# Optimization experiments

Measured on AMD Instinct MI355X. Metric: run time of the kernel, lower is better.

## Reference

```python
import jax, jax.numpy as jnp
import numpy as np

NEG_SLOPE = 0.01


def conv2d_border(x, w, b, stride):
    # replicate ('border') padding of 1, then VALID conv; matches torch padding_mode='border'
    x = jnp.pad(x, ((0, 0), (0, 0), (1, 1), (1, 1)), mode='edge')
    y = jax.lax.conv_general_dilated(x, w, (stride, stride), 'VALID',
                                     dimension_numbers=('NCHW', 'OIHW', 'NCHW'))
    return y + b[None, :, None, None]


def leaky(x):
    return jnp.where(x >= 0, x, NEG_SLOPE * x)


def view_encoder(x, w1, b1, w2, b2, w3, b3):
    x = leaky(conv2d_border(x, w1, b1, 1))
    x = leaky(conv2d_border(x, w2, b2, 2))
    x = leaky(conv2d_border(x, w3, b3, 2))
    return x  # (V, F, H/4, W/4)


def bilinear_gather(nts, uv, vid):
    # nts: (V, F, Hp, Wp); uv: (N, 2) in [0,1]; vid: (N,) int -> (N, F)
    V, Fd, Hp, Wp = nts.shape
    tex = jnp.transpose(nts, (0, 2, 3, 1))  # (V, Hp, Wp, F)
    x = uv[:, 0] * (Wp - 1)
    y = uv[:, 1] * (Hp - 1)
    x0 = jnp.clip(jnp.floor(x).astype(jnp.int32), 0, Wp - 2)
    y0 = jnp.clip(jnp.floor(y).astype(jnp.int32), 0, Hp - 2)
    wx = (x - x0)[:, None]
    wy = (y - y0)[:, None]
    f00 = tex[vid, y0, x0]
    f01 = tex[vid, y0, x0 + 1]
    f10 = tex[vid, y0 + 1, x0]
    f11 = tex[vid, y0 + 1, x0 + 1]
    return (f00 * (1 - wx) * (1 - wy) + f01 * wx * (1 - wy)
            + f10 * (1 - wx) * wy + f11 * wx * wy)


def mha(q, k, v, wq, bq, wk, bk, wv, bv, wo, bo, num_heads):
    # q: (B,1,D), k/v: (B,S,D); torch nn.MultiheadAttention math, batch_first
    B, Lq, D = q.shape
    S = k.shape[1]
    hd = D // num_heads
    qh = (q @ wq.T + bq).reshape(B, Lq, num_heads, hd).transpose(0, 2, 1, 3)
    kh = (k @ wk.T + bk).reshape(B, S, num_heads, hd).transpose(0, 2, 1, 3)
    vh = (v @ wv.T + bv).reshape(B, S, num_heads, hd).transpose(0, 2, 1, 3)
    scores = jnp.einsum('bhqd,bhkd->bhqk', qh, kh) / jnp.sqrt(jnp.float32(hd)).astype(q.dtype)
    attn = jax.nn.softmax(scores, axis=-1)
    out = jnp.einsum('bhqk,bhkd->bhqd', attn, vh)
    out = out.transpose(0, 2, 1, 3).reshape(B, Lq, D)
    return out @ wo.T + bo


def setup_inputs() -> dict:
    key = jax.random.key(0)
    ks = jax.random.split(key, 20)
    V, C, H, W = 8, 3, 512, 512
    B = 262144
    D = 64
    view_tex = jax.random.normal(ks[0], (V, C, H, W), jnp.float32)
    uv = jax.random.uniform(ks[1], (B, 3, 2), jnp.float32)
    vid = jax.random.randint(ks[2], (B, 3, 1), 0, V).astype(jnp.float32)
    uvi = jnp.concatenate([uv, vid], axis=-1)  # (B,3,3)
    raydir = jax.random.normal(ks[3], (B, 3), jnp.float32)

    def winit(k, shape, fan_in):
        return jax.random.normal(k, shape, jnp.float32) / np.sqrt(fan_in)

    params = dict(
        w1=winit(ks[4], (32, C, 3, 3), C * 9), b1=jnp.zeros((32,), jnp.float32),
        w2=winit(ks[5], (64, 32, 3, 3), 32 * 9), b2=jnp.zeros((64,), jnp.float32),
        w3=winit(ks[6], (D, 64, 3, 3), 64 * 9), b3=jnp.zeros((D,), jnp.float32),
        rw1=winit(ks[7], (64, 3), 3), rb1=jnp.zeros((64,), jnp.float32),
        rw2=winit(ks[8], (D, 64), 64), rb2=jnp.zeros((D,), jnp.float32),
        wq=winit(ks[9], (D, D), D), bq=jnp.zeros((D,), jnp.float32),
        wk=winit(ks[10], (D, D), D), bk=jnp.zeros((D,), jnp.float32),
        wv=winit(ks[11], (D, D), D), bv=jnp.zeros((D,), jnp.float32),
        wo=winit(ks[12], (D, D), D), bo=jnp.zeros((D,), jnp.float32),
    )
    return dict(view_tex=view_tex, uvi=uvi, raydir=raydir, **params)


def reference(view_tex, uvi, raydir,
              w1, b1, w2, b2, w3, b3,
              rw1, rb1, rw2, rb2,
              wq, bq, wk, bk, wv, bv, wo, bo):
    NUM_HEADS = 4
    nts = view_encoder(view_tex, w1, b1, w2, b2, w3, b3)  # (V,F,Hp,Wp)
    B = uvi.shape[0]
    uv = uvi[:, :, :2].reshape(B * 3, 2)
    vid = uvi[:, :, 2].astype(jnp.int32).reshape(B * 3)
    feats = bilinear_gather(nts, uv, vid).reshape(B, 3, -1)  # (B,3,F)
    ray_feat = jnp.maximum(raydir @ rw1.T + rb1, 0) @ rw2.T + rb2  # (B,F)
    fused = mha(ray_feat[:, None, :], feats, feats,
                wq, bq, wk, bk, wv, bv, wo, bo, NUM_HEADS)
    return fused[:, 0, :], feats
```

## Files before the change

kernel.cpp:

```cpp
#include <hip/hip_runtime.h>

typedef short s8v __attribute__((ext_vector_type(8)));
typedef short s4v __attribute__((ext_vector_type(4)));
typedef float f4v __attribute__((ext_vector_type(4)));

#define DEV __device__ __forceinline__

DEV short f2bs(float f){
  unsigned int u = __float_as_uint(f);
  u += 0x7fffu + ((u >> 16) & 1u);
  return (short)(u >> 16);
}
DEV float b2f(short s){
  return __uint_as_float(((unsigned int)(unsigned short)s) << 16);
}
DEV float lrelu(float x){ return x >= 0.f ? x : 0.01f*x; }
DEV unsigned pk2(float a, float b){
  return (unsigned)(unsigned short)f2bs(a) | ((unsigned)(unsigned short)f2bs(b) << 16);
}

__global__ __launch_bounds__(256) void k0_prep(
    const float* __restrict__ w1, const float* __restrict__ w2,
    const float* __restrict__ w3, const float* __restrict__ rw2,
    const float* __restrict__ wq, const float* __restrict__ wk,
    const float* __restrict__ wv, const float* __restrict__ wo,
    char* __restrict__ wreg)
{
  int idx = blockIdx.x*256 + threadIdx.x;
  short* w1b = (short*)(wreg);
  short* w2b = (short*)(wreg + 3456);
  short* w3b = (short*)(wreg + 40320);
  short* rw2b = (short*)(wreg + 114048);
  short* wkb  = (short*)(wreg + 130432);
  short* wvb  = (short*)(wreg + 138624);
  short* wob  = (short*)(wreg + 146816);
  if (idx < 1024){
    int e = idx & 7, l = (idx >> 3) & 63, m = idx >> 9;
    int k = (l >> 4)*8 + e;
    int cout = m*16 + (l & 15);
    w1b[idx] = (k < 27) ? f2bs(w1[cout*27 + k]) : (short)0;
  } else if (idx < 19456){
    int j = idx - 1024;
    int kk = j / 2048, c = (j >> 5) & 63, ci = j & 31;
    w2b[j] = f2bs(w2[c*288 + ci*9 + kk]);
  } else if (idx < 56320){
    int j = idx - 19456;
    int kk = j / 4096, c = (j >> 6) & 63, ci = j & 63;
    w3b[j] = f2bs(w3[c*576 + ci*9 + kk]);
  } else if (idx < 60416){
    int j = idx - 56320; rw2b[j] = f2bs(rw2[j]);
  } else if (idx < 64512){
  } else if (idx < 68608){
    int j = idx - 64512; wkb[j] = f2bs(wk[j]);
  } else if (idx < 72704){
    int j = idx - 68608; wvb[j] = f2bs(wv[j]);
  } else if (idx < 76800){
    int j = idx - 72704; wob[j] = f2bs(wo[j]);
  }
}

__global__ __launch_bounds__(256) void k0b_fold(
    const float* __restrict__ wq, const float* __restrict__ rw2,
    const float* __restrict__ rb2, const float* __restrict__ bq,
    char* __restrict__ wreg)
{
  short* wqrb = (short*)(wreg + 122240);
  float* bqr  = (float*)(wreg + 155008);
  int tid = threadIdx.x;
  int i = tid >> 2, k0 = (tid & 3)*16;
  #pragma unroll
  for (int kk=0; kk<16; kk++){
    int k = k0 + kk;
    float s = 0.f;
    #pragma unroll
    for (int j=0; j<64; j++) s += wq[i*64+j]*rw2[j*64+k];
    wqrb[i*64+k] = f2bs(s);
  }
  if (tid < 64){
    float s = bq[tid];
    #pragma unroll
    for (int j=0; j<64; j++) s += wq[tid*64+j]*rb2[j];
    bqr[tid] = s;
  }
}

__global__ __launch_bounds__(256) void kc12(
    const float* __restrict__ vt, short* __restrict__ c2,
    const short* __restrict__ w1b, const float* __restrict__ b1,
    const short* __restrict__ w2b, const float* __restrict__ b2, int v0)
{
  __shared__ short srcT[3108];
  __shared__ short rb[4][2880];
  const int tid = threadIdx.x;
  const int l = tid & 63, wid = tid >> 6;
  const int p = l & 15, g = l >> 4;
  const int yb = blockIdx.y;
  const int oyb = (yb & 7)*16 + (yb >> 3);
  const int OXB = blockIdx.x*64, OYB = oyb*2;
  const float* src = vt + (size_t)(v0 + blockIdx.z)*3*512*512;

  #pragma unroll
  for (int it=0; it<13; it++){
    int idx = it*256 + tid;
    if (idx < 3108){
      int ci = idx/1036, rem = idx - ci*1036;
      int row = rem/148, col = rem - row*148;
      int gr = min(max(2*OYB - 2 + row, 0), 511);
      int gc = min(max(2*OXB - 2 + col, 0), 511);
      srcT[idx] = f2bs(src[((size_t)ci*512 + gr)*512 + gc]);
    }
  }

  int boffB[8];
  #pragma unroll
  for (int e=0;e<8;e++){
    int k = g*8 + e;
    int ci = (k*57) >> 9;
    int r9 = k - ci*9;
    int dy = (r9*11) >> 5;
    int dx = r9 - dy*3;
    boffB[e] = (k < 27) ? (ci*1036 + dy*148 + dx) : 0;
  }
  s8v af0 = *(const s8v*)(w1b + l*8);
  s8v af1 = *(const s8v*)(w1b + 512 + l*8);
  f4v cb0 = *(const f4v*)(b1 + g*4);
  f4v cb1 = *(const f4v*)(b1 + 16 + g*4);

  const int dlt = wid >> 1, h = wid & 1;
  const int oy = OYB + dlt;
  const int ox0 = OXB + h*32;
  const int Cw0 = 2*ox0 - 1;
  short* myrb = rb[wid];
  const f4v FZ = {0.f,0.f,0.f,0.f};
  f4v acc[2][4];
  #pragma unroll
  for (int s2=0;s2<2;s2++)
    #pragma unroll
    for (int m=0;m<4;m++) acc[s2][m] = FZ;

  __syncthreads();

  #pragma unroll
  for (int ky=0; ky<3; ky++){
    const int R = min(max(2*oy + ky - 1, 0), 511);
    const int trb = R - 2*OYB + 1;
    const int sbase = trb*148 + 64*h + p;

    #pragma unroll
    for (int s=0; s<5; s++){
      s8v bf;
      #pragma unroll
      for (int e=0;e<8;e++) bf[e] = srcT[boffB[e] + sbase + s*16];
      f4v d0 = __builtin_amdgcn_mfma_f32_16x16x32_bf16(af0, bf, FZ, 0,0,0);
      f4v d1 = __builtin_amdgcn_mfma_f32_16x16x32_bf16(af1, bf, FZ, 0,0,0);
      int wcol = s*16 + p;
      uint2 wa = { pk2(lrelu(d0[0]+cb0[0]), lrelu(d0[1]+cb0[1])),
                   pk2(lrelu(d0[2]+cb0[2]), lrelu(d0[3]+cb0[3])) };
      *(uint2*)(myrb + wcol*36 + g*4) = wa;
      uint2 wb2 = { pk2(lrelu(d1[0]+cb1[0]), lrelu(d1[1]+cb1[1])),
                    pk2(lrelu(d1[2]+cb1[2]), lrelu(d1[3]+cb1[3])) };
      *(uint2*)(myrb + wcol*36 + 16 + g*4) = wb2;
    }

    #pragma unroll
    for (int s2=0; s2<2; s2++){
      const int locox = s2*16 + p;
      #pragma unroll
      for (int kx=0; kx<3; kx++){
        int raw = Cw0 + 2*locox + kx;
        int ri = max(raw, 0) - Cw0;
        uint2 lo2 = *(const uint2*)(myrb + ri*36 + g*8);
        uint2 hi2 = *(const uint2*)(myrb + ri*36 + g*8 + 4);
        uint4 t4 = {lo2.x, lo2.y, hi2.x, hi2.y};
        s8v bf2 = __builtin_bit_cast(s8v, t4);
        #pragma unroll
        for (int m=0;m<4;m++){
          s8v afr = *(const s8v*)(w2b + ((ky*3+kx)*64 + m*16 + p)*32 + g*8);
          acc[s2][m] = __builtin_amdgcn_mfma_f32_16x16x32_bf16(afr, bf2, acc[s2][m], 0,0,0);
        }
      }
    }
  }

  #pragma unroll
  for (int s2=0; s2<2; s2++){
    short* o = c2 + (((size_t)blockIdx.z*256 + oy)*256 + ox0 + s2*16 + p)*64;
    #pragma unroll
    for (int m=0;m<4;m++){
      f4v bb = *(const f4v*)(b2 + m*16 + g*4);
      s4v pk;
      #pragma unroll
      for (int r=0;r<4;r++) pk[r] = f2bs(lrelu(acc[s2][m][r] + bb[r]));
      *(s4v*)(o + m*16 + g*4) = pk;
    }
  }
}

template<int CIN, int TILES>
__global__ __launch_bounds__(256) void conv_mfma(
    const short* __restrict__ src0, short* __restrict__ dst,
    const short* __restrict__ wb, const float* __restrict__ bias,
    int IH, int IW, int OW, int dstV0)
{
  const int l = threadIdx.x & 63, w = threadIdx.x >> 6;
  const int p = l & 15, g = l >> 4;
  const int ox0 = blockIdx.x*(64*TILES) + w*(16*TILES) + p;
  const int yb = blockIdx.y;
  const int oy = (yb & 7)*16 + (yb >> 3);
  const short* src = src0 + (size_t)blockIdx.z*IH*IW*CIN;
  const f4v FZ = {0.f,0.f,0.f,0.f};
  f4v acc[TILES][4];
  #pragma unroll
  for (int tl=0;tl<TILES;tl++)
    #pragma unroll
    for (int m=0;m<4;m++) acc[tl][m] = FZ;
  #pragma unroll
  for (int ky=0;ky<3;ky++){
    int iy = min(max(2*oy+ky-1, 0), IH-1);
    #pragma unroll
    for (int kx=0;kx<3;kx++){
      #pragma unroll
      for (int ch=0; ch<CIN/32; ch++){
        s8v bfrag[TILES];
        #pragma unroll
        for (int tl=0;tl<TILES;tl++){
          int ix = min(max(2*(ox0 + 16*tl)+kx-1, 0), IW-1);
          bfrag[tl] = *(const s8v*)(src + ((size_t)iy*IW + ix)*CIN + ch*32 + g*8);
        }
        #pragma unroll
        for (int m=0;m<4;m++){
          s8v afrag = *(const s8v*)(wb + ((ky*3+kx)*64 + m*16 + p)*CIN + ch*32 + g*8);
          #pragma unroll
          for (int tl=0;tl<TILES;tl++)
            acc[tl][m] = __builtin_amdgcn_mfma_f32_16x16x32_bf16(afrag, bfrag[tl], acc[tl][m], 0,0,0);
        }
      }
    }
  }
  const int OH = gridDim.y;
  #pragma unroll
  for (int tl=0;tl<TILES;tl++){
    short* o = dst + (((size_t)(dstV0 + blockIdx.z)*OH + oy)*OW + ox0 + 16*tl)*64;
    #pragma unroll
    for (int m=0;m<4;m++){
      f4v bb = *(const f4v*)(bias + m*16 + g*4);
      s4v pk;
      #pragma unroll
      for (int r=0;r<4;r++) pk[r] = f2bs(lrelu(acc[tl][m][r] + bb[r]));
      *(s4v*)(o + m*16 + g*4) = pk;
    }
  }
}

#define AFRG(W) (*(const s8v*)((W) + (m*16 + p)*64 + kc*32 + g*8))

__global__ __launch_bounds__(256) void k45_fused(
    const short* __restrict__ nts, const float* __restrict__ uvi,
    const float* __restrict__ raydir,
    const float* __restrict__ rw1, const float* __restrict__ rb1,
    const short* __restrict__ wqrb, const float* __restrict__ bqr,
    const short* __restrict__ wkb, const float* __restrict__ bk,
    const short* __restrict__ wvb, const float* __restrict__ bv,
    const short* __restrict__ wob, const float* __restrict__ bo,
    float* __restrict__ outFused, float* __restrict__ outFeats)
{
  __shared__ short lds_fb[64*3*72];
  const int tid = threadIdx.x;
  const int l = tid & 63, wid = tid >> 6;
  const int p = l & 15, g = l >> 4;
  const int pt0 = blockIdx.x*64;
  const f4v FZ = {0.f,0.f,0.f,0.f};

  #pragma unroll
  for (int i=0; i<6; i++){
    int ck = i*256 + tid;
    int ptl = ck/24, rem = ck - ptl*24;
    int t = rem >> 3, c8 = rem & 7;
    int pt = pt0 + ptl;
    const float* up = uvi + (size_t)pt*9 + t*3;
    float u = up[0], v = up[1];
    int vid = (int)up[2];
    float xf = u*127.f, yf = v*127.f;
    int x0 = min(max((int)floorf(xf), 0), 126);
    int y0 = min(max((int)floorf(yf), 0), 126);
    float wx = xf - (float)x0, wy = yf - (float)y0;
    const short* cb = nts + ((size_t)((vid*128 + y0)*128 + x0))*64 + c8*8;
    s8v c00 = *(const s8v*)(cb);
    s8v c01 = *(const s8v*)(cb + 64);
    s8v c10 = *(const s8v*)(cb + 8192);
    s8v c11 = *(const s8v*)(cb + 8192 + 64);
    f4v o0, o1;
    s8v pk;
    #pragma unroll
    for (int e=0;e<8;e++){
      float a = b2f(c00[e]); a += wx*(b2f(c01[e]) - a);
      float b = b2f(c10[e]); b += wx*(b2f(c11[e]) - b);
      float val = a + wy*(b - a);
      if (e < 4) o0[e] = val; else o1[e-4] = val;
      pk[e] = f2bs(val);
    }
    float* op = outFeats + ((size_t)pt*3 + t)*64 + c8*8;
    *(f4v*)op = o0;
    *(f4v*)(op+4) = o1;
    *(s8v*)(&lds_fb[(ptl*3 + t)*72 + c8*8]) = pk;
  }

  __syncthreads();

  const int ptl16 = wid*16 + p;
  const int pt = pt0 + ptl16;

  s8v fb[3][2];
  #pragma unroll
  for (int t=0;t<3;t++)
    #pragma unroll
    for (int kc=0;kc<2;kc++)
      fb[t][kc] = *(const s8v*)(&lds_fb[(ptl16*3 + t)*72 + kc*32 + g*8]);

  float rd0 = raydir[(size_t)pt*3+0];
  float rd1 = raydir[(size_t)pt*3+1];
  float rd2 = raydir[(size_t)pt*3+2];
  s8v xb[2];
  #pragma unroll
  for (int kc=0;kc<2;kc++){
    s8v tmp;
    #pragma unroll
    for (int e=0;e<8;e++){
      int j = kc*32 + g*8 + e;
      float hv = fmaxf(rb1[j] + rw1[j*3]*rd0 + rw1[j*3+1]*rd1 + rw1[j*3+2]*rd2, 0.f);
      tmp[e] = f2bs(hv);
    }
    xb[kc] = tmp;
  }

  f4v acc[4];
  #pragma unroll
  for (int m=0;m<4;m++) acc[m] = FZ;
  #pragma unroll
  for (int kc=0;kc<2;kc++){
    #pragma unroll
    for (int m=0;m<4;m++)
      acc[m] = __builtin_amdgcn_mfma_f32_16x16x32_bf16(AFRG(wqrb), xb[kc], acc[m], 0,0,0);
  }
  float qh[4][4];
  #pragma unroll
  for (int m=0;m<4;m++){
    f4v bb = *(const f4v*)(bqr + m*16 + g*4);
    #pragma unroll
    for (int r=0;r<4;r++) qh[m][r] = acc[m][r] + bb[r];
  }

  s8v wkf[2][4];
  #pragma unroll
  for (int kc=0;kc<2;kc++)
    #pragma unroll
    for (int m=0;m<4;m++)
      wkf[kc][m] = AFRG(wkb);

  float sc[3][4];
  #pragma unroll
  for (int t=0;t<3;t++){
    f4v ka[4];
    #pragma unroll
    for (int m=0;m<4;m++) ka[m] = FZ;
    #pragma unroll
    for (int kc=0;kc<2;kc++){
      #pragma unroll
      for (int m=0;m<4;m++)
        ka[m] = __builtin_amdgcn_mfma_f32_16x16x32_bf16(wkf[kc][m], fb[t][kc], ka[m], 0,0,0);
    }
    #pragma unroll
    for (int m=0;m<4;m++){
      f4v bb = *(const f4v*)(bk + m*16 + g*4);
      float part = 0.f;
      #pragma unroll
      for (int r=0;r<4;r++) part += qh[m][r]*(ka[m][r] + bb[r]);
      part += __shfl_xor(part, 16, 64);
      part += __shfl_xor(part, 32, 64);
      sc[t][m] = part*0.25f;
    }
  }

  #pragma unroll
  for (int m=0;m<4;m++){
    float mx = fmaxf(fmaxf(sc[0][m], sc[1][m]), sc[2][m]);
    float e0 = __expf(sc[0][m]-mx);
    float e1 = __expf(sc[1][m]-mx);
    float e2 = __expf(sc[2][m]-mx);
    float inv = 1.f/(e0+e1+e2);
    sc[0][m] = e0*inv; sc[1][m] = e1*inv; sc[2][m] = e2*inv;
  }

  s8v wvf[2][4];
  #pragma unroll
  for (int kc=0;kc<2;kc++)
    #pragma unroll
    for (int m=0;m<4;m++)
      wvf[kc][m] = AFRG(wvb);

  float o[4][4];
  #pragma unroll
  for (int m=0;m<4;m++)
    #pragma unroll
    for (int r=0;r<4;r++) o[m][r] = 0.f;
  #pragma unroll
  for (int t=0;t<3;t++){
    f4v va[4];
    #pragma unroll
    for (int m=0;m<4;m++) va[m] = FZ;
    #pragma unroll
    for (int kc=0;kc<2;kc++){
      #pragma unroll
      for (int m=0;m<4;m++)
        va[m] = __builtin_amdgcn_mfma_f32_16x16x32_bf16(wvf[kc][m], fb[t][kc], va[m], 0,0,0);
    }
    #pragma unroll
    for (int m=0;m<4;m++)
      #pragma unroll
      for (int r=0;r<4;r++) o[m][r] += sc[t][m]*va[m][r];
  }
  #pragma unroll
  for (int m=0;m<4;m++){
    f4v bb = *(const f4v*)(bv + m*16 + g*4);
    #pragma unroll
    for (int r=0;r<4;r++) o[m][r] += bb[r];
  }

  {
    unsigned* rl = (unsigned*)lds_fb + wid*1728;
    #pragma unroll
    for (int m=0;m<4;m++){
      unsigned lo = pk2(o[m][0], o[m][1]);
      unsigned hi = pk2(o[m][2], o[m][3]);
      rl[p*36 + m*8 + g*2] = lo;
      rl[p*36 + m*8 + g*2 + 1] = hi;
    }
    xb[0] = __builtin_bit_cast(s8v, *(uint4*)(rl + p*36 + g*4));
    xb[1] = __builtin_bit_cast(s8v, *(uint4*)(rl + p*36 + 16 + g*4));
  }

  #pragma unroll
  for (int m=0;m<4;m++) acc[m] = FZ;
  #pragma unroll
  for (int kc=0;kc<2;kc++){
    #pragma unroll
    for (int m=0;m<4;m++)
      acc[m] = __builtin_amdgcn_mfma_f32_16x16x32_bf16(AFRG(wob), xb[kc], acc[m], 0,0,0);
  }
  #pragma unroll
  for (int m=0;m<4;m++){
    f4v bb = *(const f4v*)(bo + m*16 + g*4);
    f4v res;
    #pragma unroll
    for (int r=0;r<4;r++) res[r] = acc[m][r] + bb[r];
    *(f4v*)(outFused + (size_t)pt*64 + m*16 + g*4) = res;
  }
}

extern "C" void kernel_launch(void* const* d_in, const int* in_sizes, int n_in,
                              void* d_out, int out_size, void* d_ws, size_t ws_size,
                              hipStream_t stream)
{
  const float* view_tex = (const float*)d_in[0];
  const float* uvi    = (const float*)d_in[1];
  const float* raydir = (const float*)d_in[2];
  const float* w1 = (const float*)d_in[3];
  const float* b1 = (const float*)d_in[4];
  const float* w2 = (const float*)d_in[5];
  const float* b2 = (const float*)d_in[6];
  const float* w3 = (const float*)d_in[7];
  const float* b3 = (const float*)d_in[8];
  const float* rw1 = (const float*)d_in[9];
  const float* rb1 = (const float*)d_in[10];
  const float* rw2 = (const float*)d_in[11];
  const float* rb2 = (const float*)d_in[12];
  const float* wq = (const float*)d_in[13];
  const float* bq = (const float*)d_in[14];
  const float* wk = (const float*)d_in[15];
  const float* bk = (const float*)d_in[16];
  const float* wv = (const float*)d_in[17];
  const float* bv = (const float*)d_in[18];
  const float* wo = (const float*)d_in[19];
  const float* bo = (const float*)d_in[20];
  float* out = (float*)d_out;

  const int V = in_sizes[0] / (3*512*512);
  const int B = in_sizes[1] / 9;
  const size_t FEATS_OFF = (size_t)B*64;

  const size_t C2F  = (size_t)V*256*256*64*2;
  const size_t C2V  = (size_t)256*256*64*2;
  const size_t NTSB = (size_t)V*128*128*64*2;
  const size_t WREG = 262144;

  char* base = (char*)d_ws;
  bool full = (ws_size >= C2F + NTSB + WREG);

  char *c2, *ntsp, *wreg;
  if (full){
    c2 = base; ntsp = c2 + C2F; wreg = ntsp + NTSB;
  } else {
    c2 = base; ntsp = c2 + C2V; wreg = ntsp + NTSB;
  }
  short* w1b = (short*)(wreg);
  short* w2b = (short*)(wreg + 3456);
  short* w3b = (short*)(wreg + 40320);
  short* wqrb = (short*)(wreg + 122240);
  short* wkb  = (short*)(wreg + 130432);
  short* wvb  = (short*)(wreg + 138624);
  short* wob  = (short*)(wreg + 146816);
  float* bqr  = (float*)(wreg + 155008);

  k0_prep<<<dim3(300),256,0,stream>>>(w1,w2,w3,rw2,wq,wk,wv,wo,wreg);
  k0b_fold<<<dim3(1),256,0,stream>>>(wq, rw2, rb2, bq, wreg);

  if (full){
    kc12<<<dim3(4,128,V),256,0,stream>>>(view_tex,(short*)c2,w1b,b1,w2b,b2,0);
    conv_mfma<64,2><<<dim3(1,128,V),256,0,stream>>>((const short*)c2,(short*)ntsp,w3b,b3,256,256,128,0);
  } else {
    for (int v=0; v<V; v++){
      kc12<<<dim3(4,128,1),256,0,stream>>>(view_tex,(short*)c2,w1b,b1,w2b,b2,v);
      conv_mfma<64,2><<<dim3(1,128,1),256,0,stream>>>((const short*)c2,(short*)ntsp,w3b,b3,256,256,128,v);
    }
  }

  k45_fused<<<dim3(B/64),256,0,stream>>>((const short*)ntsp, uvi, raydir,
      rw1, rb1, wqrb, bqr, wkb, bk, wvb, bv, wob, bo,
      out, out + FEATS_OFF);
}
```

Before: 308.1 us.

## Sort gather tokens by view via counting sort before bilinear gather

Splits the fused gather+attention kernel into a counting-sort pass (histogram, offsets, scatter) that groups gather tokens by view id, a view-ordered bilinear gather kernel with block swizzling, and a separate attention kernel that reloads the fp32 features from global memory. The aim is better cache locality on the texture feature map during gathers. In exchange it adds several extra launches, atomics, and a round-trip of the feature tensor through global memory. The fallback path for small workspaces now always runs the full-size conv, so it is no longer memory-safe, and the scatter order is nondeterministic.

```diff
diff --git a/kernel.cpp b/kernel.cpp
--- a/kernel.cpp
+++ b/kernel.cpp
@@ -84,6 +84,87 @@
   }
 }
 
+__global__ void kzero(int* cnt){ if (threadIdx.x < 8) cnt[threadIdx.x] = 0; }
+
+__global__ __launch_bounds__(256) void kcnt(
+    const float* __restrict__ uvi, int* __restrict__ cnt)
+{
+  __shared__ int lh[8];
+  int tid = threadIdx.x;
+  if (tid < 8) lh[tid] = 0;
+  __syncthreads();
+  int tk = blockIdx.x*256 + tid;
+  int v = (int)uvi[(size_t)tk*3 + 2];
+  atomicAdd(&lh[v], 1);
+  __syncthreads();
+  if (tid < 8) atomicAdd(&cnt[tid], lh[tid]);
+}
+
+__global__ void kofs(const int* cnt, int* cur)
+{
+  if (threadIdx.x == 0){
+    int run = 0;
+    for (int v=0; v<8; v++){ cur[v] = run; run += cnt[v]; }
+  }
+}
+
+__global__ __launch_bounds__(256) void kscat(
+    const float* __restrict__ uvi, int* __restrict__ cur,
+    int* __restrict__ ord, float2* __restrict__ uvo)
+{
+  __shared__ int lh[8];
+  __shared__ int gb[8];
+  int tid = threadIdx.x;
+  if (tid < 8) lh[tid] = 0;
+  __syncthreads();
+  int tk = blockIdx.x*256 + tid;
+  float u = uvi[(size_t)tk*3];
+  float vv = uvi[(size_t)tk*3 + 1];
+  int v = (int)uvi[(size_t)tk*3 + 2];
+  int rank = atomicAdd(&lh[v], 1);
+  __syncthreads();
+  if (tid < 8) gb[tid] = atomicAdd(&cur[tid], lh[tid]);
+  __syncthreads();
+  int pos = gb[v] + rank;
+  ord[pos] = tk;
+  uvo[pos] = make_float2(u, vv);
+}
+
+__global__ __launch_bounds__(256) void k4v(
+    const short* __restrict__ nts, const int* __restrict__ ord,
+    const float2* __restrict__ uvo, float* __restrict__ outFeats, int nblk8)
+{
+  int b = blockIdx.x;
+  int swb = (b & 7)*nblk8 + (b >> 3);
+  int tid = threadIdx.x;
+  int idx = swb*32 + (tid >> 3);
+  int c8 = tid & 7;
+  int tok = ord[idx];
+  float2 uv = uvo[idx];
+  float xf = uv.x*127.f, yf = uv.y*127.f;
+  int x0 = min(max((int)floorf(xf), 0), 126);
+  int y0 = min(max((int)floorf(yf), 0), 126);
+  float wx = xf - (float)x0, wy = yf - (float)y0;
+  int vid = tok >> 24;
+  tok &= 0xFFFFFF;
+  const short* cb = nts + ((size_t)((vid*128 + y0)*128 + x0))*64 + c8*8;
+  s8v c00 = *(const s8v*)(cb);
+  s8v c01 = *(const s8v*)(cb + 64);
+  s8v c10 = *(const s8v*)(cb + 8192);
+  s8v c11 = *(const s8v*)(cb + 8192 + 64);
+  f4v o0, o1;
+  #pragma unroll
+  for (int e=0;e<8;e++){
+    float a = b2f(c00[e]); a += wx*(b2f(c01[e]) - a);
+    float b2 = b2f(c10[e]); b2 += wx*(b2f(c11[e]) - b2);
+    float val = a + wy*(b2 - a);
+    if (e < 4) o0[e] = val; else o1[e-4] = val;
+  }
+  float* op = outFeats + (size_t)tok*64 + c8*8;
+  *(f4v*)op = o0;
+  *(f4v*)(op+4) = o1;
+}
+
 __global__ __launch_bounds__(256) void kc12(
     const float* __restrict__ vt, short* __restrict__ c2,
     const short* __restrict__ w1b, const float* __restrict__ b1,
@@ -254,68 +335,36 @@
 
 #define AFRG(W) (*(const s8v*)((W) + (m*16 + p)*64 + kc*32 + g*8))
 
-__global__ __launch_bounds__(256) void k45_fused(
-    const short* __restrict__ nts, const float* __restrict__ uvi,
-    const float* __restrict__ raydir,
+__global__ __launch_bounds__(256) void k5s(
+    const float* __restrict__ feats, const float* __restrict__ raydir,
     const float* __restrict__ rw1, const float* __restrict__ rb1,
     const short* __restrict__ wqrb, const float* __restrict__ bqr,
     const short* __restrict__ wkb, const float* __restrict__ bk,
     const short* __restrict__ wvb, const float* __restrict__ bv,
     const short* __restrict__ wob, const float* __restrict__ bo,
-    float* __restrict__ outFused, float* __restrict__ outFeats)
-{
-  __shared__ short lds_fb[64*3*72];
+    float* __restrict__ outFused)
+{
+  __shared__ unsigned rlds[4][576];
   const int tid = threadIdx.x;
   const int l = tid & 63, wid = tid >> 6;
   const int p = l & 15, g = l >> 4;
-  const int pt0 = blockIdx.x*64;
+  const int pt = blockIdx.x*64 + wid*16 + p;
   const f4v FZ = {0.f,0.f,0.f,0.f};
 
-  #pragma unroll
-  for (int i=0; i<6; i++){
-    int ck = i*256 + tid;
-    int ptl = ck/24, rem = ck - ptl*24;
-    int t = rem >> 3, c8 = rem & 7;
-    int pt = pt0 + ptl;
-    const float* up = uvi + (size_t)pt*9 + t*3;
-    float u = up[0], v = up[1];
-    int vid = (int)up[2];
-    float xf = u*127.f, yf = v*127.f;
-    int x0 = min(max((int)floorf(xf), 0), 126);
-    int y0 = min(max((int)floorf(yf), 0), 126);
-    float wx = xf - (float)x0, wy = yf - (float)y0;
-    const short* cb = nts + ((size_t)((vid*128 + y0)*128 + x0))*64 + c8*8;
-    s8v c00 = *(const s8v*)(cb);
-    s8v c01 = *(const s8v*)(cb + 64);
-    s8v c10 = *(const s8v*)(cb + 8192);
-    s8v c11 = *(const s8v*)(cb + 8192 + 64);
-    f4v o0, o1;
-    s8v pk;
-    #pragma unroll
-    for (int e=0;e<8;e++){
-      float a = b2f(c00[e]); a += wx*(b2f(c01[e]) - a);
-      float b = b2f(c10[e]); b += wx*(b2f(c11[e]) - b);
-      float val = a + wy*(b - a);
-      if (e < 4) o0[e] = val; else o1[e-4] = val;
-      pk[e] = f2bs(val);
-    }
-    float* op = outFeats + ((size_t)pt*3 + t)*64 + c8*8;
-    *(f4v*)op = o0;
-    *(f4v*)(op+4) = o1;
-    *(s8v*)(&lds_fb[(ptl*3 + t)*72 + c8*8]) = pk;
-  }
-
-  __syncthreads();
-
-  const int ptl16 = wid*16 + p;
-  const int pt = pt0 + ptl16;
-
   s8v fb[3][2];
   #pragma unroll
-  for (int t=0;t<3;t++)
-    #pragma unroll
-    for (int kc=0;kc<2;kc++)
-      fb[t][kc] = *(const s8v*)(&lds_fb[(ptl16*3 + t)*72 + kc*32 + g*8]);
+  for (int t=0;t<3;t++){
+    const float* fp = feats + (size_t)(pt*3+t)*64;
+    #pragma unroll
+    for (int kc=0;kc<2;kc++){
+      f4v a0 = *(const f4v*)(fp + kc*32 + g*8);
+      f4v a1 = *(const f4v*)(fp + kc*32 + g*8 + 4);
+      s8v tmp;
+      #pragma unroll
+      for (int e=0;e<4;e++){ tmp[e] = f2bs(a0[e]); tmp[e+4] = f2bs(a1[e]); }
+      fb[t][kc] = tmp;
+    }
+  }
 
   float rd0 = raydir[(size_t)pt*3+0];
   float rd1 = raydir[(size_t)pt*3+1];
@@ -427,7 +476,7 @@
   }
 
   {
-    unsigned* rl = (unsigned*)lds_fb + wid*1728;
+    unsigned* rl = rlds[wid];
     #pragma unroll
     for (int m=0;m<4;m++){
       unsigned lo = pk2(o[m][0], o[m][1]);
@@ -455,6 +504,28 @@
     for (int r=0;r<4;r++) res[r] = acc[m][r] + bb[r];
     *(f4v*)(outFused + (size_t)pt*64 + m*16 + g*4) = res;
   }
+}
+
+__global__ __launch_bounds__(256) void kscat2(
+    const float* __restrict__ uvi, int* __restrict__ cur,
+    int* __restrict__ ord, float2* __restrict__ uvo)
+{
+  __shared__ int lh[8];
+  __shared__ int gb[8];
+  int tid = threadIdx.x;
+  if (tid < 8) lh[tid] = 0;
+  __syncthreads();
+  int tk = blockIdx.x*256 + tid;
+  float u = uvi[(size_t)tk*3];
+  float vv = uvi[(size_t)tk*3 + 1];
+  int v = (int)uvi[(size_t)tk*3 + 2];
+  int rank = atomicAdd(&lh[v], 1);
+  __syncthreads();
+  if (tid < 8) gb[tid] = atomicAdd(&cur[tid], lh[tid]);
+  __syncthreads();
+  int pos = gb[v] + rank;
+  ord[pos] = tk | (v << 24);
+  uvo[pos] = make_float2(u, vv);
 }
 
 extern "C" void kernel_launch(void* const* d_in, const int* in_sizes, int n_in,
@@ -486,22 +557,27 @@
 
   const int V = in_sizes[0] / (3*512*512);
   const int B = in_sizes[1] / 9;
+  const int B3 = B*3;
   const size_t FEATS_OFF = (size_t)B*64;
 
   const size_t C2F  = (size_t)V*256*256*64*2;
-  const size_t C2V  = (size_t)256*256*64*2;
   const size_t NTSB = (size_t)V*128*128*64*2;
   const size_t WREG = 262144;
+  const size_t ORDB = (size_t)B3*4;
+  const size_t UVOB = (size_t)B3*8;
+  const size_t CNTB = 256;
 
   char* base = (char*)d_ws;
-  bool full = (ws_size >= C2F + NTSB + WREG);
-
-  char *c2, *ntsp, *wreg;
-  if (full){
-    c2 = base; ntsp = c2 + C2F; wreg = ntsp + NTSB;
-  } else {
-    c2 = base; ntsp = c2 + C2V; wreg = ntsp + NTSB;
-  }
+  bool full = (ws_size >= C2F + NTSB + WREG + ORDB + UVOB + CNTB);
+
+  char* c2   = base;
+  char* ntsp = c2 + C2F;
+  char* wreg = ntsp + NTSB;
+  int*    ord = (int*)(wreg + WREG);
+  float2* uvo = (float2*)((char*)ord + ORDB);
+  int*    cnt = (int*)((char*)uvo + UVOB);
+  int*    cur = cnt + 8;
+
   short* w1b = (short*)(wreg);
   short* w2b = (short*)(wreg + 3456);
   short* w3b = (short*)(wreg + 40320);
@@ -514,17 +590,27 @@
   k0_prep<<<dim3(300),256,0,stream>>>(w1,w2,w3,rw2,wq,wk,wv,wo,wreg);
   k0b_fold<<<dim3(1),256,0,stream>>>(wq, rw2, rb2, bq, wreg);
 
+  kc12<<<dim3(4,128,V),256,0,stream>>>(view_tex,(short*)c2,w1b,b1,w2b,b2,0);
+  conv_mfma<64,2><<<dim3(1,128,V),256,0,stream>>>((const short*)c2,(short*)ntsp,w3b,b3,256,256,128,0);
+
   if (full){
-    kc12<<<dim3(4,128,V),256,0,stream>>>(view_tex,(short*)c2,w1b,b1,w2b,b2,0);
-    conv_mfma<64,2><<<dim3(1,128,V),256,0,stream>>>((const short*)c2,(short*)ntsp,w3b,b3,256,256,128,0);
+    kzero<<<dim3(1),64,0,stream>>>(cnt);
+    kcnt<<<dim3(B3/256),256,0,stream>>>(uvi, cnt);
+    kofs<<<dim3(1),64,0,stream>>>(cnt, cur);
+    kscat2<<<dim3(B3/256),256,0,stream>>>(uvi, cur, ord, uvo);
+    int nblk = (B3*8)/256;
+    k4v<<<dim3(nblk),256,0,stream>>>((const short*)ntsp, ord, uvo,
+        out + FEATS_OFF, nblk/8);
   } else {
-    for (int v=0; v<V; v++){
-      kc12<<<dim3(4,128,1),256,0,stream>>>(view_tex,(short*)c2,w1b,b1,w2b,b2,v);
-      conv_mfma<64,2><<<dim3(1,128,1),256,0,stream>>>((const short*)c2,(short*)ntsp,w3b,b3,256,256,128,v);
-    }
-  }
-
-  k45_fused<<<dim3(B/64),256,0,stream>>>((const short*)ntsp, uvi, raydir,
-      rw1, rb1, wqrb, bqr, wkb, bk, wvb, bv, wob, bo,
-      out, out + FEATS_OFF);
-}
+    kzero<<<dim3(1),64,0,stream>>>(cnt);
+    kcnt<<<dim3(B3/256),256,0,stream>>>(uvi, cnt);
+    kofs<<<dim3(1),64,0,stream>>>(cnt, cur);
+    kscat2<<<dim3(B3/256),256,0,stream>>>(uvi, cur, ord, uvo);
+    int nblk = (B3*8)/256;
+    k4v<<<dim3(nblk),256,0,stream>>>((const short*)ntsp, ord, uvo,
+        out + FEATS_OFF, nblk/8);
+  }
+
+  k5s<<<dim3(B/64),256,0,stream>>>(out + FEATS_OFF, raydir,
+      rw1, rb1, wqrb, bqr, wkb, bk, wvb, bv, wob, bo, out);
+}
```

Result: slower. 403.4 us (+30.9%).
